# Kernel tuning notes

Hardware: AMD Instinct MI355X
Metric: run time of the kernel (lower is better)

Reference implementation:

```python
import jax, jax.numpy as jnp
import numpy as np

B, I, H = 4096, 1024, 2048
EPS = 1e-5  # nn.GroupNorm default eps


def setup_inputs() -> dict:
    key = jax.random.key(0)
    ks = jax.random.split(key, 16)
    s_in = 1.0 / np.sqrt(I)
    s_h = 1.0 / np.sqrt(H)
    inp = {
        "x": jax.random.normal(ks[0], (B, I), jnp.float32),
        "h_prev": jax.random.normal(ks[1], (B, H), jnp.float32),
        "c_prev": jax.random.normal(ks[2], (B, H), jnp.float32),
        "n_prev": jnp.ones((B, H), jnp.float32),
        "m_prev": jax.random.normal(ks[3], (B, H), jnp.float32),
        # W_* : Linear(I, H) weight [H, I] + bias [H]
        "Wi": jax.random.uniform(ks[4], (H, I), jnp.float32, -s_in, s_in),
        "Wf": jax.random.uniform(ks[5], (H, I), jnp.float32, -s_in, s_in),
        "Wz": jax.random.uniform(ks[6], (H, I), jnp.float32, -s_in, s_in),
        "Wo": jax.random.uniform(ks[7], (H, I), jnp.float32, -s_in, s_in),
        "bi": jax.random.uniform(ks[8], (H,), jnp.float32, -s_in, s_in),
        "bf": jax.random.uniform(ks[9], (H,), jnp.float32, -s_in, s_in),
        "bz": jax.random.uniform(ks[10], (H,), jnp.float32, -s_in, s_in),
        "bo": jax.random.uniform(ks[11], (H,), jnp.float32, -s_in, s_in),
        # R_* : Linear(H, H, bias=False) weight [H, H]
        "Ri": jax.random.uniform(ks[12], (H, H), jnp.float32, -s_h, s_h),
        "Rf": jax.random.uniform(ks[13], (H, H), jnp.float32, -s_h, s_h),
        "Rz": jax.random.uniform(ks[14], (H, H), jnp.float32, -s_h, s_h),
        "Ro": jax.random.uniform(ks[15], (H, H), jnp.float32, -s_h, s_h),
        # GroupNorm(1, H) affine params
        "gn_w": jnp.ones((H,), jnp.float32),
        "gn_b": jnp.zeros((H,), jnp.float32),
    }
    return inp


def _group_norm1(x, w, b):
    # GroupNorm with 1 group on [B, H]: normalize over all H per sample
    mu = jnp.mean(x, axis=-1, keepdims=True)
    var = jnp.mean(jnp.square(x - mu), axis=-1, keepdims=True)
    return (x - mu) * jax.lax.rsqrt(var + EPS) * w + b


def reference(x, h_prev, c_prev, n_prev, m_prev,
              Wi, Wf, Wz, Wo, bi, bf, bz, bo,
              Ri, Rf, Rz, Ro, gn_w, gn_b):
    # Batch the 4 input and 4 recurrent GEMMs into one each: [B, 4H]
    Wcat = jnp.concatenate([Wi, Wf, Wz, Wo], axis=0)   # [4H, I]
    bcat = jnp.concatenate([bi, bf, bz, bo], axis=0)   # [4H]
    Rcat = jnp.concatenate([Ri, Rf, Rz, Ro], axis=0)   # [4H, H]
    pre = x @ Wcat.T + bcat + h_prev @ Rcat.T          # [B, 4H]
    pi, pf, pz, po = jnp.split(pre, 4, axis=-1)
    i = jax.nn.sigmoid(pi)
    f = jax.nn.sigmoid(pf)
    z = jnp.tanh(pz)
    o = jax.nn.sigmoid(po)
    m = jnp.maximum(f * m_prev, i)
    c = f * c_prev + i * z
    n = f * n_prev + i
    c_stab = c / n
    h = o * jnp.tanh(_group_norm1(c_stab, gn_w, gn_b))
    return (h, c, n, m)
```

## Files before the change

kernel.cpp:

```cpp
#include <hip/hip_runtime.h>
#include <hip/hip_bf16.h>
#include <math.h>

#define B_ 4096
#define I_ 1024
#define H_ 2048
#define K_ 3072
#define N4 8192
#define EPSGN 1e-5f

#define NT_K 48
#define PANB 16384
#define LDSB 65536

typedef __bf16 bf16;
typedef __bf16 bf16x8 __attribute__((ext_vector_type(8)));
typedef float  f32x4  __attribute__((ext_vector_type(4)));

__device__ __forceinline__ float sigm(float x) {
  return 1.0f / (1.0f + __expf(-x));
}
__device__ __forceinline__ float tanh_fast(float x) {
  float a = fabsf(x);
  float e = __expf(-2.0f * a);
  float t = (1.0f - e) / (1.0f + e);
  return copysignf(t, x);
}

__global__ void convA(const float* __restrict__ x, const float* __restrict__ hp,
                      char* __restrict__ At) {
  int sid = blockIdx.x * blockDim.x + threadIdx.x;
  int p = sid & 1023;
  int pan = sid >> 10;
  int mt = pan / 96;
  int rem = pan - mt * 96;
  int kt = rem >> 1;
  int h = rem & 1;
  int r = p >> 3;
  int ks = (p & 7) ^ (r & 7);
  int row = mt * 256 + h * 128 + r;
  int k = kt * 64 + ks * 8;
  const float* src = (k < I_) ? (x + (size_t)row * I_ + k)
                              : (hp + (size_t)row * H_ + (k - I_));
  f32x4 v0 = *(const f32x4*)src;
  f32x4 v1 = *(const f32x4*)(src + 4);
  bf16x8 o;
  o[0]=(bf16)v0[0]; o[1]=(bf16)v0[1]; o[2]=(bf16)v0[2]; o[3]=(bf16)v0[3];
  o[4]=(bf16)v1[0]; o[5]=(bf16)v1[1]; o[6]=(bf16)v1[2]; o[7]=(bf16)v1[3];
  *(bf16x8*)(At + (size_t)sid * 16) = o;
}

__global__ void convB(const float* __restrict__ Wi, const float* __restrict__ Wf,
                      const float* __restrict__ Wz, const float* __restrict__ Wo,
                      const float* __restrict__ Ri, const float* __restrict__ Rf,
                      const float* __restrict__ Rz, const float* __restrict__ Ro,
                      char* __restrict__ Bt) {
  int sid = blockIdx.x * blockDim.x + threadIdx.x;
  int p = sid & 1023;
  int pan = sid >> 10;
  int nt = pan / 96;
  int rem = pan - nt * 96;
  int kt = rem >> 1;
  int h = rem & 1;
  int r = p >> 3;
  int ks = (p & 7) ^ (r & 7);
  int n = nt * 256 + h * 128 + r;
  int g = n >> 11;
  int hr = n & 2047;
  int k = kt * 64 + ks * 8;
  const float* Wp = (g == 0) ? Wi : (g == 1) ? Wf : (g == 2) ? Wz : Wo;
  const float* Rp = (g == 0) ? Ri : (g == 1) ? Rf : (g == 2) ? Rz : Ro;
  const float* src = (k < I_) ? (Wp + (size_t)hr * I_ + k)
                              : (Rp + (size_t)hr * H_ + (k - I_));
  f32x4 v0 = *(const f32x4*)src;
  f32x4 v1 = *(const f32x4*)(src + 4);
  bf16x8 o;
  o[0]=(bf16)v0[0]; o[1]=(bf16)v0[1]; o[2]=(bf16)v0[2]; o[3]=(bf16)v0[3];
  o[4]=(bf16)v1[0]; o[5]=(bf16)v1[1]; o[6]=(bf16)v1[2]; o[7]=(bf16)v1[3];
  *(bf16x8*)(Bt + (size_t)sid * 16) = o;
}

__device__ __forceinline__ void gload16(const char* g, char* l) {
  __builtin_amdgcn_global_load_lds(
      (const __attribute__((address_space(1))) void*)g,
      (__attribute__((address_space(3))) void*)l, 16, 0, 0);
}
__device__ __forceinline__ void stage(const char* g, char* l) {
  gload16(g, l);
  gload16(g + 8192, l + 8192);
}

__global__ __launch_bounds__(512, 2) void gemm8(const char* __restrict__ At,
                                                const char* __restrict__ Bt,
                                                bf16* __restrict__ pre) {
  extern __shared__ char lds[];
  const int tid = threadIdx.x;
  const int lane = tid & 63;
  const int wv = tid >> 6;
  const int wm = wv >> 2;
  const int wn = wv & 3;

  int bid = (blockIdx.x & 7) * 64 + (blockIdx.x >> 3);
  const int bm = bid >> 5;
  const int bn = bid & 31;

  const char* a_src = At + (size_t)bm * (NT_K * 2 * PANB) + tid * 16;
  const char* b_src = Bt + (size_t)bn * (NT_K * 2 * PANB) + tid * 16;
  char* a_lds = lds + tid * 16;
  char* b_lds = lds + LDSB + tid * 16;

  const int l15 = lane & 15;
  const int l7  = lane & 7;
  const int q   = lane >> 4;
  int offk[2];
  offk[0] = l15 * 128 + (((0 + q) ^ l7) << 4);
  offk[1] = l15 * 128 + (((4 + q) ^ l7) << 4);

  const char* apan_base = lds + wm * PANB;
  const char* bpan_base = lds + LDSB + (wn >> 1) * PANB;
  const int bcol = (wn & 1) * 8192;

  f32x4 acc[8][4] = {};
  bf16x8 af[4][2];
  bf16x8 bn0[2][2];
  bf16x8 bn1[2][2];

  stage(b_src + 0 * PANB, b_lds + 0 * PANB);
  stage(b_src + 1 * PANB, b_lds + 1 * PANB);
  stage(a_src + 0 * PANB, a_lds + 0 * PANB);
  stage(a_src + 1 * PANB, a_lds + 1 * PANB);
  stage(b_src + 2 * PANB, b_lds + 2 * PANB);
  stage(b_src + 3 * PANB, b_lds + 3 * PANB);
  asm volatile("s_waitcnt vmcnt(4)" ::: "memory");
  __builtin_amdgcn_s_barrier();

#pragma unroll
  for (int mi = 0; mi < 4; ++mi)
#pragma unroll
    for (int ks = 0; ks < 2; ++ks)
      af[mi][ks] = *(const bf16x8*)(apan_base + mi * 2048 + offk[ks]);
#pragma unroll
  for (int nj = 0; nj < 2; ++nj)
#pragma unroll
    for (int ks = 0; ks < 2; ++ks)
      bn0[nj][ks] = *(const bf16x8*)(bpan_base + bcol + nj * 2048 + offk[ks]);

#pragma unroll 2
  for (int t = 0; t < NT_K; ++t) {
    const int par = (t & 1) * 2;
    const char* apan  = apan_base + par * PANB;
    const char* bpan  = bpan_base + par * PANB;
    const char* apanN = apan_base + (2 - par) * PANB;
    const char* bpanN = bpan_base + (2 - par) * PANB;

    __builtin_amdgcn_s_setprio(1);
#pragma unroll
    for (int mi = 0; mi < 4; ++mi)
#pragma unroll
      for (int nj = 0; nj < 2; ++nj)
#pragma unroll
        for (int ks = 0; ks < 2; ++ks)
          acc[mi][nj] = __builtin_amdgcn_mfma_f32_16x16x32_bf16(
              af[mi][ks], bn0[nj][ks], acc[mi][nj], 0, 0, 0);
    __builtin_amdgcn_s_setprio(0);
    if (t + 1 < NT_K)
      stage(a_src + (size_t)(t + 1) * 2 * PANB, a_lds + (2 - par) * PANB);
#pragma unroll
    for (int nj = 0; nj < 2; ++nj)
#pragma unroll
      for (int ks = 0; ks < 2; ++ks)
        bn1[nj][ks] = *(const bf16x8*)(bpan + bcol + 4096 + nj * 2048 + offk[ks]);
    __builtin_amdgcn_s_barrier();

    __builtin_amdgcn_s_setprio(1);
#pragma unroll
    for (int mi = 0; mi < 4; ++mi)
#pragma unroll
      for (int nj = 0; nj < 2; ++nj)
#pragma unroll
        for (int ks = 0; ks < 2; ++ks)
          acc[mi][2 + nj] = __builtin_amdgcn_mfma_f32_16x16x32_bf16(
              af[mi][ks], bn1[nj][ks], acc[mi][2 + nj], 0, 0, 0);
    __builtin_amdgcn_s_setprio(0);
    if (t + 1 < NT_K)
      stage(a_src + (size_t)(t + 1) * 2 * PANB + PANB, a_lds + (3 - par) * PANB);
#pragma unroll
    for (int mi = 0; mi < 4; ++mi)
#pragma unroll
      for (int ks = 0; ks < 2; ++ks)
        af[mi][ks] = *(const bf16x8*)(apan + 8192 + mi * 2048 + offk[ks]);
    __builtin_amdgcn_s_barrier();

    __builtin_amdgcn_s_setprio(1);
#pragma unroll
    for (int mi = 0; mi < 4; ++mi)
#pragma unroll
      for (int nj = 0; nj < 2; ++nj)
#pragma unroll
        for (int ks = 0; ks < 2; ++ks)
          acc[4 + mi][2 + nj] = __builtin_amdgcn_mfma_f32_16x16x32_bf16(
              af[mi][ks], bn1[nj][ks], acc[4 + mi][2 + nj], 0, 0, 0);
    __builtin_amdgcn_s_setprio(0);
    if (t + 2 < NT_K)
      stage(b_src + (size_t)(t + 2) * 2 * PANB, b_lds + par * PANB);
    if (t < NT_K - 2)
      asm volatile("s_waitcnt vmcnt(2)" ::: "memory");
    else
      asm volatile("s_waitcnt vmcnt(0)" ::: "memory");
    __builtin_amdgcn_s_barrier();

    __builtin_amdgcn_s_setprio(1);
#pragma unroll
    for (int mi = 0; mi < 4; ++mi)
#pragma unroll
      for (int nj = 0; nj < 2; ++nj)
#pragma unroll
        for (int ks = 0; ks < 2; ++ks)
          acc[4 + mi][nj] = __builtin_amdgcn_mfma_f32_16x16x32_bf16(
              af[mi][ks], bn0[nj][ks], acc[4 + mi][nj], 0, 0, 0);
    __builtin_amdgcn_s_setprio(0);
    if (t + 2 < NT_K)
      stage(b_src + (size_t)(t + 2) * 2 * PANB + PANB, b_lds + (par + 1) * PANB);
    if (t + 1 < NT_K) {
#pragma unroll
      for (int mi = 0; mi < 4; ++mi)
#pragma unroll
        for (int ks = 0; ks < 2; ++ks)
          af[mi][ks] = *(const bf16x8*)(apanN + mi * 2048 + offk[ks]);
#pragma unroll
      for (int nj = 0; nj < 2; ++nj)
#pragma unroll
        for (int ks = 0; ks < 2; ++ks)
          bn0[nj][ks] = *(const bf16x8*)(bpanN + bcol + nj * 2048 + offk[ks]);
    }
    __builtin_amdgcn_s_barrier();
  }

  const int crow0 = (lane >> 4) * 4;
  const int ccol  = lane & 15;
#pragma unroll
  for (int mi = 0; mi < 8; ++mi)
#pragma unroll
    for (int nj = 0; nj < 4; ++nj)
#pragma unroll
      for (int j = 0; j < 4; ++j) {
        int row = bm * 256 + wm * 128 + mi * 16 + crow0 + j;
        int col = bn * 256 + wn * 64 + nj * 16 + ccol;
        pre[(size_t)row * N4 + col] = (bf16)acc[mi][nj][j];
      }
}

__global__ __launch_bounds__(256) void fusedpost(
    const bf16* __restrict__ pre,
    const float* __restrict__ bi, const float* __restrict__ bfp,
    const float* __restrict__ bz, const float* __restrict__ bo,
    const float* __restrict__ c_prev, const float* __restrict__ n_prev,
    const float* __restrict__ m_prev,
    const float* __restrict__ gnw, const float* __restrict__ gnb,
    float* __restrict__ out) {
  const int b = blockIdx.x;
  const int t = threadIdx.x;
  const int h0 = t * 8;
  const long PL = (long)B_ * H_;
  const long e = (long)b * H_ + h0;
  const bf16* prow = pre + (size_t)b * N4;

  bf16x8 PI = *(const bf16x8*)(prow + 0 * H_ + h0);
  bf16x8 PF = *(const bf16x8*)(prow + 1 * H_ + h0);
  bf16x8 PZ = *(const bf16x8*)(prow + 2 * H_ + h0);
  bf16x8 PO = *(const bf16x8*)(prow + 3 * H_ + h0);
  f32x4 BI0 = *(const f32x4*)(bi + h0),  BI1 = *(const f32x4*)(bi + h0 + 4);
  f32x4 BF0 = *(const f32x4*)(bfp + h0), BF1 = *(const f32x4*)(bfp + h0 + 4);
  f32x4 BZ0 = *(const f32x4*)(bz + h0),  BZ1 = *(const f32x4*)(bz + h0 + 4);
  f32x4 BO0 = *(const f32x4*)(bo + h0),  BO1 = *(const f32x4*)(bo + h0 + 4);
  f32x4 CP0 = *(const f32x4*)(c_prev + e), CP1 = *(const f32x4*)(c_prev + e + 4);
  f32x4 NP0 = *(const f32x4*)(n_prev + e), NP1 = *(const f32x4*)(n_prev + e + 4);
  f32x4 MP0 = *(const f32x4*)(m_prev + e), MP1 = *(const f32x4*)(m_prev + e + 4);

  float cs[8], og[8];
  f32x4 C0, C1, N0, N1, M0, M1;
  float sum = 0.f, sq = 0.f;
#pragma unroll
  for (int j = 0; j < 8; ++j) {
    float pi = (float)PI[j] + ((j < 4) ? BI0[j] : BI1[j - 4]);
    float pf = (float)PF[j] + ((j < 4) ? BF0[j] : BF1[j - 4]);
    float pz = (float)PZ[j] + ((j < 4) ? BZ0[j] : BZ1[j - 4]);
    float po = (float)PO[j] + ((j < 4) ? BO0[j] : BO1[j - 4]);
    float cp = (j < 4) ? CP0[j] : CP1[j - 4];
    float np = (j < 4) ? NP0[j] : NP1[j - 4];
    float mp = (j < 4) ? MP0[j] : MP1[j - 4];
    float ig = sigm(pi);
    float fg = sigm(pf);
    float zg = tanh_fast(pz);
    og[j] = sigm(po);
    float m = fmaxf(fg * mp, ig);
    float c = fg * cp + ig * zg;
    float n = fg * np + ig;
    if (j < 4) { C0[j] = c; N0[j] = n; M0[j] = m; }
    else       { C1[j-4] = c; N1[j-4] = n; M1[j-4] = m; }
    float v = c / n;
    cs[j] = v;
    sum += v;
    sq  += v * v;
  }
  *(f32x4*)(out + PL * 1 + e) = C0; *(f32x4*)(out + PL * 1 + e + 4) = C1;
  *(f32x4*)(out + PL * 2 + e) = N0; *(f32x4*)(out + PL * 2 + e + 4) = N1;
  *(f32x4*)(out + PL * 3 + e) = M0; *(f32x4*)(out + PL * 3 + e + 4) = M1;

#pragma unroll
  for (int off = 1; off < 64; off <<= 1) {
    sum += __shfl_xor(sum, off);
    sq  += __shfl_xor(sq, off);
  }
  __shared__ float s1[4], s2[4];
  const int wv = t >> 6, lane = t & 63;
  if (lane == 0) { s1[wv] = sum; s2[wv] = sq; }
  __syncthreads();
  sum = s1[0] + s1[1] + s1[2] + s1[3];
  sq  = s2[0] + s2[1] + s2[2] + s2[3];
  const float mu  = sum * (1.0f / H_);
  const float var = sq * (1.0f / H_) - mu * mu;
  const float rinv = rsqrtf(var + EPSGN);

  f32x4 GW0 = *(const f32x4*)(gnw + h0), GW1 = *(const f32x4*)(gnw + h0 + 4);
  f32x4 GB0 = *(const f32x4*)(gnb + h0), GB1 = *(const f32x4*)(gnb + h0 + 4);
  f32x4 Hh0, Hh1;
#pragma unroll
  for (int j = 0; j < 8; ++j) {
    float gw = (j < 4) ? GW0[j] : GW1[j - 4];
    float gb = (j < 4) ? GB0[j] : GB1[j - 4];
    float g = (cs[j] - mu) * rinv * gw + gb;
    float hv = og[j] * tanh_fast(g);
    if (j < 4) Hh0[j] = hv; else Hh1[j - 4] = hv;
  }
  *(f32x4*)(out + e) = Hh0;
  *(f32x4*)(out + e + 4) = Hh1;
}

extern "C" void kernel_launch(void* const* d_in, const int* in_sizes, int n_in,
                              void* d_out, int out_size, void* d_ws, size_t ws_size,
                              hipStream_t stream) {
  const float* x      = (const float*)d_in[0];
  const float* h_prev = (const float*)d_in[1];
  const float* c_prev = (const float*)d_in[2];
  const float* n_prev = (const float*)d_in[3];
  const float* m_prev = (const float*)d_in[4];
  const float* Wi = (const float*)d_in[5];
  const float* Wf = (const float*)d_in[6];
  const float* Wz = (const float*)d_in[7];
  const float* Wo = (const float*)d_in[8];
  const float* bi = (const float*)d_in[9];
  const float* bf = (const float*)d_in[10];
  const float* bz = (const float*)d_in[11];
  const float* bo = (const float*)d_in[12];
  const float* Ri = (const float*)d_in[13];
  const float* Rf = (const float*)d_in[14];
  const float* Rz = (const float*)d_in[15];
  const float* Ro = (const float*)d_in[16];
  const float* gnw = (const float*)d_in[17];
  const float* gnb = (const float*)d_in[18];

  char* ws = (char*)d_ws;
  char* At = ws;
  char* Bt = ws + (size_t)B_ * K_ * 2;
  bf16* pre = (bf16*)(ws + (size_t)B_ * K_ * 2 + (size_t)N4 * K_ * 2);
  float* out = (float*)d_out;

  hipFuncSetAttribute((const void*)gemm8,
                      hipFuncAttributeMaxDynamicSharedMemorySize, 131072);

  convA<<<((size_t)B_ * K_ / 8) / 256, 256, 0, stream>>>(x, h_prev, At);
  convB<<<((size_t)N4 * K_ / 8) / 256, 256, 0, stream>>>(Wi, Wf, Wz, Wo,
                                                         Ri, Rf, Rz, Ro, Bt);
  gemm8<<<512, 512, 131072, stream>>>(At, Bt, pre);
  fusedpost<<<B_, 256, 0, stream>>>(pre, bi, bf, bz, bo,
                                    c_prev, n_prev, m_prev, gnw, gnb, out);
}
```

Before: 286.8 us.

## Shrink GEMM tile to 128x256 with BK=32 and triple-buffered LDS pipeline

Restructures the bf16 GEMM from 256x256 tiles with BK=64 and double buffering to 128x256 tiles with BK=32, a three-stage LDS ring and a smaller swizzle. The pre-tiled layouts produced by convA and convB are changed to match. The goal is more blocks (1024) and more waves per CU through lower LDS use and fewer accumulators, which should hide latency better. In exchange, A-reuse per loaded B drops and the number of barriers per unit of K work doubles.

```diff
diff --git a/kernel.cpp b/kernel.cpp
--- a/kernel.cpp
+++ b/kernel.cpp
@@ -9,9 +9,10 @@
 #define N4 8192
 #define EPSGN 1e-5f
 
-#define NT_K 48
-#define PANB 16384
-#define LDSB 65536
+#define NT_K 96
+#define APAN 8192
+#define BPAN 16384
+#define B_OFF 24576
 
 typedef __bf16 bf16;
 typedef __bf16 bf16x8 __attribute__((ext_vector_type(8)));
@@ -30,16 +31,14 @@
 __global__ void convA(const float* __restrict__ x, const float* __restrict__ hp,
                       char* __restrict__ At) {
   int sid = blockIdx.x * blockDim.x + threadIdx.x;
-  int p = sid & 1023;
-  int pan = sid >> 10;
+  int p = sid & 511;
+  int pan = sid >> 9;
   int mt = pan / 96;
-  int rem = pan - mt * 96;
-  int kt = rem >> 1;
-  int h = rem & 1;
-  int r = p >> 3;
-  int ks = (p & 7) ^ (r & 7);
-  int row = mt * 256 + h * 128 + r;
-  int k = kt * 64 + ks * 8;
+  int kt = pan - mt * 96;
+  int r = p >> 2;
+  int ks = (p & 3) ^ ((r >> 1) & 3);
+  int row = mt * 128 + r;
+  int k = kt * 32 + ks * 8;
   const float* src = (k < I_) ? (x + (size_t)row * I_ + k)
                               : (hp + (size_t)row * H_ + (k - I_));
   f32x4 v0 = *(const f32x4*)src;
@@ -56,18 +55,18 @@
                       const float* __restrict__ Rz, const float* __restrict__ Ro,
                       char* __restrict__ Bt) {
   int sid = blockIdx.x * blockDim.x + threadIdx.x;
-  int p = sid & 1023;
-  int pan = sid >> 10;
-  int nt = pan / 96;
-  int rem = pan - nt * 96;
-  int kt = rem >> 1;
-  int h = rem & 1;
-  int r = p >> 3;
-  int ks = (p & 7) ^ (r & 7);
+  int p = sid & 511;
+  int pan = sid >> 9;
+  int h = pan & 1;
+  int pk = pan >> 1;
+  int nt = pk / 96;
+  int kt = pk - nt * 96;
+  int r = p >> 2;
+  int ks = (p & 3) ^ ((r >> 1) & 3);
   int n = nt * 256 + h * 128 + r;
   int g = n >> 11;
   int hr = n & 2047;
-  int k = kt * 64 + ks * 8;
+  int k = kt * 32 + ks * 8;
   const float* Wp = (g == 0) ? Wi : (g == 1) ? Wf : (g == 2) ? Wz : Wo;
   const float* Rp = (g == 0) ? Ri : (g == 1) ? Rf : (g == 2) ? Rz : Ro;
   const float* src = (k < I_) ? (Wp + (size_t)hr * I_ + k)
@@ -85,12 +84,8 @@
       (const __attribute__((address_space(1))) void*)g,
       (__attribute__((address_space(3))) void*)l, 16, 0, 0);
 }
-__device__ __forceinline__ void stage(const char* g, char* l) {
-  gload16(g, l);
-  gload16(g + 8192, l + 8192);
-}
-
-__global__ __launch_bounds__(512, 2) void gemm8(const char* __restrict__ At,
+
+__global__ __launch_bounds__(512, 4) void gemm8(const char* __restrict__ At,
                                                 const char* __restrict__ Bt,
                                                 bf16* __restrict__ pre) {
   extern __shared__ char lds[];
@@ -100,138 +95,85 @@
   const int wm = wv >> 2;
   const int wn = wv & 3;
 
-  int bid = (blockIdx.x & 7) * 64 + (blockIdx.x >> 3);
+  int bid = (blockIdx.x & 7) * 128 + (blockIdx.x >> 3);
   const int bm = bid >> 5;
   const int bn = bid & 31;
 
-  const char* a_src = At + (size_t)bm * (NT_K * 2 * PANB) + tid * 16;
-  const char* b_src = Bt + (size_t)bn * (NT_K * 2 * PANB) + tid * 16;
+  const char* a_src = At + (size_t)bm * (NT_K * APAN) + tid * 16;
+  const char* b_src = Bt + (size_t)bn * (NT_K * BPAN) + tid * 16;
   char* a_lds = lds + tid * 16;
-  char* b_lds = lds + LDSB + tid * 16;
+  char* b_lds = lds + B_OFF + tid * 16;
 
   const int l15 = lane & 15;
-  const int l7  = lane & 7;
   const int q   = lane >> 4;
-  int offk[2];
-  offk[0] = l15 * 128 + (((0 + q) ^ l7) << 4);
-  offk[1] = l15 * 128 + (((4 + q) ^ l7) << 4);
-
-  const char* apan_base = lds + wm * PANB;
-  const char* bpan_base = lds + LDSB + (wn >> 1) * PANB;
-  const int bcol = (wn & 1) * 8192;
-
-  f32x4 acc[8][4] = {};
-  bf16x8 af[4][2];
-  bf16x8 bn0[2][2];
-  bf16x8 bn1[2][2];
-
-  stage(b_src + 0 * PANB, b_lds + 0 * PANB);
-  stage(b_src + 1 * PANB, b_lds + 1 * PANB);
-  stage(a_src + 0 * PANB, a_lds + 0 * PANB);
-  stage(a_src + 1 * PANB, a_lds + 1 * PANB);
-  stage(b_src + 2 * PANB, b_lds + 2 * PANB);
-  stage(b_src + 3 * PANB, b_lds + 3 * PANB);
-  asm volatile("s_waitcnt vmcnt(4)" ::: "memory");
+  const int loff = l15 * 64 + ((q ^ ((l15 >> 1) & 3)) << 4);
+  const int aoff = wm * 4096 + loff;
+  const int boff = (wn >> 1) * 8192 + (wn & 1) * 4096 + loff;
+  const char* aL = lds;
+  const char* bL = lds + B_OFF;
+
+  f32x4 acc[4][4] = {};
+  bf16x8 af[4], b0[2], b1[2];
+
+  gload16(a_src + 0 * APAN, a_lds + 0 * APAN);
+  gload16(b_src + 0 * BPAN, b_lds + 0 * BPAN);
+  gload16(b_src + 0 * BPAN + 8192, b_lds + 0 * BPAN + 8192);
+  gload16(a_src + 1 * APAN, a_lds + 1 * APAN);
+  gload16(b_src + 1 * BPAN, b_lds + 1 * BPAN);
+  gload16(b_src + 1 * BPAN + 8192, b_lds + 1 * BPAN + 8192);
+  asm volatile("s_waitcnt vmcnt(3)" ::: "memory");
   __builtin_amdgcn_s_barrier();
 
 #pragma unroll
   for (int mi = 0; mi < 4; ++mi)
-#pragma unroll
-    for (int ks = 0; ks < 2; ++ks)
-      af[mi][ks] = *(const bf16x8*)(apan_base + mi * 2048 + offk[ks]);
+    af[mi] = *(const bf16x8*)(aL + 0 * APAN + aoff + mi * 1024);
 #pragma unroll
   for (int nj = 0; nj < 2; ++nj)
-#pragma unroll
-    for (int ks = 0; ks < 2; ++ks)
-      bn0[nj][ks] = *(const bf16x8*)(bpan_base + bcol + nj * 2048 + offk[ks]);
-
-#pragma unroll 2
+    b0[nj] = *(const bf16x8*)(bL + 0 * BPAN + boff + nj * 1024);
+
+#pragma unroll 3
   for (int t = 0; t < NT_K; ++t) {
-    const int par = (t & 1) * 2;
-    const char* apan  = apan_base + par * PANB;
-    const char* bpan  = bpan_base + par * PANB;
-    const char* apanN = apan_base + (2 - par) * PANB;
-    const char* bpanN = bpan_base + (2 - par) * PANB;
-
+    const int sC = t % 3;
+    const int sN = (t + 1) % 3;
+    const int sP = (t + 2) % 3;
+    if (t + 2 < NT_K)
+      gload16(a_src + (size_t)(t + 2) * APAN, a_lds + sP * APAN);
     __builtin_amdgcn_s_setprio(1);
 #pragma unroll
     for (int mi = 0; mi < 4; ++mi)
 #pragma unroll
       for (int nj = 0; nj < 2; ++nj)
-#pragma unroll
-        for (int ks = 0; ks < 2; ++ks)
-          acc[mi][nj] = __builtin_amdgcn_mfma_f32_16x16x32_bf16(
-              af[mi][ks], bn0[nj][ks], acc[mi][nj], 0, 0, 0);
+        acc[mi][nj] = __builtin_amdgcn_mfma_f32_16x16x32_bf16(
+            af[mi], b0[nj], acc[mi][nj], 0, 0, 0);
     __builtin_amdgcn_s_setprio(0);
-    if (t + 1 < NT_K)
-      stage(a_src + (size_t)(t + 1) * 2 * PANB, a_lds + (2 - par) * PANB);
 #pragma unroll
     for (int nj = 0; nj < 2; ++nj)
-#pragma unroll
-      for (int ks = 0; ks < 2; ++ks)
-        bn1[nj][ks] = *(const bf16x8*)(bpan + bcol + 4096 + nj * 2048 + offk[ks]);
-    __builtin_amdgcn_s_barrier();
-
-    __builtin_amdgcn_s_setprio(1);
-#pragma unroll
-    for (int mi = 0; mi < 4; ++mi)
-#pragma unroll
-      for (int nj = 0; nj < 2; ++nj)
-#pragma unroll
-        for (int ks = 0; ks < 2; ++ks)
-          acc[mi][2 + nj] = __builtin_amdgcn_mfma_f32_16x16x32_bf16(
-              af[mi][ks], bn1[nj][ks], acc[mi][2 + nj], 0, 0, 0);
-    __builtin_amdgcn_s_setprio(0);
-    if (t + 1 < NT_K)
-      stage(a_src + (size_t)(t + 1) * 2 * PANB + PANB, a_lds + (3 - par) * PANB);
-#pragma unroll
-    for (int mi = 0; mi < 4; ++mi)
-#pragma unroll
-      for (int ks = 0; ks < 2; ++ks)
-        af[mi][ks] = *(const bf16x8*)(apan + 8192 + mi * 2048 + offk[ks]);
-    __builtin_amdgcn_s_barrier();
-
-    __builtin_amdgcn_s_setprio(1);
-#pragma unroll
-    for (int mi = 0; mi < 4; ++mi)
-#pragma unroll
-      for (int nj = 0; nj < 2; ++nj)
-#pragma unroll
-        for (int ks = 0; ks < 2; ++ks)
-          acc[4 + mi][2 + nj] = __builtin_amdgcn_mfma_f32_16x16x32_bf16(
-              af[mi][ks], bn1[nj][ks], acc[4 + mi][2 + nj], 0, 0, 0);
-    __builtin_amdgcn_s_setprio(0);
-    if (t + 2 < NT_K)
-      stage(b_src + (size_t)(t + 2) * 2 * PANB, b_lds + par * PANB);
+      b1[nj] = *(const bf16x8*)(bL + sC * BPAN + boff + (2 + nj) * 1024);
     if (t < NT_K - 2)
-      asm volatile("s_waitcnt vmcnt(2)" ::: "memory");
+      asm volatile("s_waitcnt vmcnt(1)" ::: "memory");
     else
       asm volatile("s_waitcnt vmcnt(0)" ::: "memory");
     __builtin_amdgcn_s_barrier();
 
+    if (t + 2 < NT_K) {
+      gload16(b_src + (size_t)(t + 2) * BPAN, b_lds + sP * BPAN);
+      gload16(b_src + (size_t)(t + 2) * BPAN + 8192, b_lds + sP * BPAN + 8192);
+    }
     __builtin_amdgcn_s_setprio(1);
 #pragma unroll
     for (int mi = 0; mi < 4; ++mi)
 #pragma unroll
       for (int nj = 0; nj < 2; ++nj)
-#pragma unroll
-        for (int ks = 0; ks < 2; ++ks)
-          acc[4 + mi][nj] = __builtin_amdgcn_mfma_f32_16x16x32_bf16(
-              af[mi][ks], bn0[nj][ks], acc[4 + mi][nj], 0, 0, 0);
+        acc[mi][2 + nj] = __builtin_amdgcn_mfma_f32_16x16x32_bf16(
+            af[mi], b1[nj], acc[mi][2 + nj], 0, 0, 0);
     __builtin_amdgcn_s_setprio(0);
-    if (t + 2 < NT_K)
-      stage(b_src + (size_t)(t + 2) * 2 * PANB + PANB, b_lds + (par + 1) * PANB);
     if (t + 1 < NT_K) {
 #pragma unroll
       for (int mi = 0; mi < 4; ++mi)
-#pragma unroll
-        for (int ks = 0; ks < 2; ++ks)
-          af[mi][ks] = *(const bf16x8*)(apanN + mi * 2048 + offk[ks]);
+        af[mi] = *(const bf16x8*)(aL + sN * APAN + aoff + mi * 1024);
 #pragma unroll
       for (int nj = 0; nj < 2; ++nj)
-#pragma unroll
-        for (int ks = 0; ks < 2; ++ks)
-          bn0[nj][ks] = *(const bf16x8*)(bpanN + bcol + nj * 2048 + offk[ks]);
+        b0[nj] = *(const bf16x8*)(bL + sN * BPAN + boff + nj * 1024);
     }
     __builtin_amdgcn_s_barrier();
   }
@@ -239,12 +181,12 @@
   const int crow0 = (lane >> 4) * 4;
   const int ccol  = lane & 15;
 #pragma unroll
-  for (int mi = 0; mi < 8; ++mi)
+  for (int mi = 0; mi < 4; ++mi)
 #pragma unroll
     for (int nj = 0; nj < 4; ++nj)
 #pragma unroll
       for (int j = 0; j < 4; ++j) {
-        int row = bm * 256 + wm * 128 + mi * 16 + crow0 + j;
+        int row = bm * 128 + wm * 64 + mi * 16 + crow0 + j;
         int col = bn * 256 + wn * 64 + nj * 16 + ccol;
         pre[(size_t)row * N4 + col] = (bf16)acc[mi][nj][j];
       }
@@ -367,12 +309,12 @@
   float* out = (float*)d_out;
 
   hipFuncSetAttribute((const void*)gemm8,
-                      hipFuncAttributeMaxDynamicSharedMemorySize, 131072);
+                      hipFuncAttributeMaxDynamicSharedMemorySize, 73728);
 
   convA<<<((size_t)B_ * K_ / 8) / 256, 256, 0, stream>>>(x, h_prev, At);
   convB<<<((size_t)N4 * K_ / 8) / 256, 256, 0, stream>>>(Wi, Wf, Wz, Wo,
                                                          Ri, Rf, Rz, Ro, Bt);
-  gemm8<<<512, 512, 131072, stream>>>(At, Bt, pre);
+  gemm8<<<1024, 512, 73728, stream>>>(At, Bt, pre);
   fusedpost<<<B_, 256, 0, stream>>>(pre, bi, bf, bz, bo,
                                     c_prev, n_prev, m_prev, gnw, gnb, out);
 }
```

After: 339.6 us. 18.4% more time.
